# Kernel optimization log

Measured on AMD Instinct MI355X. Metric: run time of the kernel, lower is better.

## Reference

```python
import jax, jax.numpy as jnp
import numpy as np

Q = 400          # num queries
P = 200000       # num points in event
N_INST = 100     # num GT instances
ALPHA = 0.25     # focal alpha
GAMMA = 2.0      # focal gamma
COST_MASK_W = 1.0
COST_DICE_W = 1.0


def setup_inputs() -> dict:
    key = jax.random.key(0)
    k1, k2 = jax.random.split(key)
    pred_masks = jax.random.normal(k1, (Q, P), dtype=jnp.float32)
    labels = jax.random.randint(k2, (P,), 0, N_INST, dtype=jnp.int64 if jax.config.jax_enable_x64 else jnp.int32)
    return {"pred_masks": pred_masks, "labels": labels, "num_instances": N_INST}


def reference(pred_masks, labels, num_instances):
    # pred_masks: [Q, P] mask logits; labels: [P] instance ids in [0, num_instances)
    x = pred_masks.astype(jnp.float32)
    p = jax.nn.sigmoid(x)                      # [Q, P]
    log_p = jax.nn.log_sigmoid(x)              # log sigmoid(x), stable
    log_1mp = jax.nn.log_sigmoid(-x)           # log(1 - sigmoid(x)), stable

    # Focal BCE per point, split by binary target value t in {0,1}:
    #   t=1: alpha     * (1-p)^gamma * (-log p)
    #   t=0: (1-alpha) *    p^gamma  * (-log(1-p))
    f1 = -ALPHA * (1.0 - p) ** GAMMA * log_p        # [Q, P]
    f0 = -(1.0 - ALPHA) * p ** GAMMA * log_1mp      # [Q, P]

    # One-hot GT masks per instance: T[p, j] = 1 iff labels[p] == j
    T = jax.nn.one_hot(labels, num_instances, dtype=jnp.float32)  # [P, N]

    # cost_mask[q, j] = mean_p [ T[p,j]*f1[q,p] + (1-T[p,j])*f0[q,p] ]
    #                 = ( (f1 - f0) @ T + sum_p f0 ) / P   -- avoids [Q,N,P]
    Pn = jnp.asarray(x.shape[1], dtype=jnp.float32)
    cost_mask = (jnp.einsum('qp,pj->qj', f1 - f0, T) + f0.sum(-1, keepdims=True)) / Pn

    # Dice cost (same einsum form as the torch code)
    counts = T.sum(0)                                # [N] points per instance
    numerator = 2.0 * jnp.einsum('qp,pj->qj', p, T)  # [Q, N]
    denominator = p.sum(-1)[:, None] + counts[None, :]
    cost_dice = 1.0 - (numerator + 1.0) / (denominator + 1.0)

    return COST_MASK_W * cost_mask + COST_DICE_W * cost_dice  # [Q, N]
```

## Files before the change

### kernel.cpp

```cpp
#include <hip/hip_runtime.h>
#include <hip/hip_bf16.h>
#include <cstdint>


#define FOCAL_ALPHA 0.25f
constexpr int NMAX   = 128;
constexpr int NTILES = 7;
constexpr int BLOCK  = 256;
constexpr int KC     = 110;

typedef __attribute__((ext_vector_type(8))) short short8;
typedef __attribute__((ext_vector_type(4))) float f32x4;

__device__ __forceinline__ void point_math(float x, float& d, float& f0o, float& po) {
    float e  = __expf(-x);
    float a  = 1.0f + e;
    float p  = __builtin_amdgcn_rcpf(a);
    float l  = __logf(a);
    float lm = -x - l;
    float om = e * p;
    float f1 = FOCAL_ALPHA * (om * om) * l;
    float f0 = -(1.0f - FOCAL_ALPHA) * (p * p) * lm;
    d   = f1 - f0;
    f0o = f0;
    po  = p;
}

__device__ __forceinline__ uint32_t pack_bf16_trunc(float lo, float hi) {
    return __builtin_amdgcn_perm(__float_as_uint(hi), __float_as_uint(lo), 0x07060302u);
}

__global__ __launch_bounds__(256) void
build_B(const int* __restrict__ labels, uint4* __restrict__ Bpre, int steps) {
    int tid  = blockIdx.x * 256 + threadIdx.x;
    int step = tid >> 6;
    int lane = tid & 63;
    if (step >= steps) return;
    const int quad = lane >> 4;
    const int m    = lane & 15;
    const int base = step * 32 + quad * 8;
    int4 l0 = *(const int4*)(labels + base);
    int4 l1 = *(const int4*)(labels + base + 4);
    int ls[8] = {l0.x, l0.y, l0.z, l0.w, l1.x, l1.y, l1.z, l1.w};
    #pragma unroll
    for (int t = 0; t < NTILES; ++t) {
        const int tgt = t * 16 + m;
        uint32_t u[4];
        #pragma unroll
        for (int i = 0; i < 4; ++i) {
            uint32_t lo = (ls[2*i]   == tgt) ? 0x00003F80u : 0u;
            uint32_t hi = (ls[2*i+1] == tgt) ? 0x3F800000u : 0u;
            u[i] = lo | hi;
        }
        Bpre[((size_t)step * NTILES + t) * 64 + lane] = make_uint4(u[0], u[1], u[2], u[3]);
    }
}

union BU { uint4 q; short8 v; uint32_t u[4]; };

__global__ __launch_bounds__(BLOCK) void
matcher_main_pre(const float* __restrict__ pred, const uint4* __restrict__ Bpre,
                 float* __restrict__ S1, float* __restrict__ S2,
                 float* __restrict__ sumf0, float* __restrict__ sump,
                 int Q, int P, int N) {
    const int tid  = threadIdx.x;
    const int wave = tid >> 6;
    const int lane = tid & 63;
    const int m    = lane & 15;
    const int quad = lane >> 4;

    const int strip = blockIdx.y * 4 + wave;
    const int q0    = strip * 16;
    if (q0 >= Q) return;

    const int total_steps = P >> 5;
    const int per         = (total_steps + KC - 1) / KC;
    const int s0          = blockIdx.x * per;
    const int s1          = min(s0 + per, total_steps);
    if (s0 >= s1) return;

    const float* pr = pred + (size_t)(q0 + m) * P + quad * 8 + s0 * 32;
    const uint4* bp = Bpre + (size_t)s0 * (NTILES * 64) + lane;

    f32x4 c1[NTILES], c2[NTILES];
    #pragma unroll
    for (int t = 0; t < NTILES; ++t) {
        c1[t] = (f32x4){0.f, 0.f, 0.f, 0.f};
        c2[t] = (f32x4){0.f, 0.f, 0.f, 0.f};
    }
    float sf0 = 0.0f, sp = 0.0f;

    float4 cx0 = *(const float4*)pr;
    float4 cx1 = *(const float4*)(pr + 4);
    BU cb[NTILES];
    #pragma unroll
    for (int t = 0; t < NTILES; ++t) cb[t].q = bp[t * 64];

    for (int s = s0; s < s1; ++s) {
        pr += 32; bp += NTILES * 64;
        float4 nx0, nx1; BU nb[NTILES];
        if (s + 1 < s1) {
            nx0 = *(const float4*)pr;
            nx1 = *(const float4*)(pr + 4);
            #pragma unroll
            for (int t = 0; t < NTILES; ++t) nb[t].q = bp[t * 64];
        }

        float xs[8] = {cx0.x, cx0.y, cx0.z, cx0.w, cx1.x, cx1.y, cx1.z, cx1.w};
        float v[8], pv[8];
        #pragma unroll
        for (int j = 0; j < 8; ++j) {
            float f0j;
            point_math(xs[j], v[j], f0j, pv[j]);
            sf0 += f0j;
            sp  += pv[j];
        }

        BU A1, A2;
        #pragma unroll
        for (int i = 0; i < 4; ++i) {
            A1.u[i] = pack_bf16_trunc(v[2*i],  v[2*i+1]);
            A2.u[i] = pack_bf16_trunc(pv[2*i], pv[2*i+1]);
        }

        #pragma unroll
        for (int t = 0; t < NTILES; ++t) {
            c1[t] = __builtin_amdgcn_mfma_f32_16x16x32_bf16(A1.v, cb[t].v, c1[t], 0, 0, 0);
            c2[t] = __builtin_amdgcn_mfma_f32_16x16x32_bf16(A2.v, cb[t].v, c2[t], 0, 0, 0);
        }

        cx0 = nx0; cx1 = nx1;
        #pragma unroll
        for (int t = 0; t < NTILES; ++t) cb[t] = nb[t];
    }

    sf0 += __shfl_xor(sf0, 16, 64);
    sf0 += __shfl_xor(sf0, 32, 64);
    sp  += __shfl_xor(sp, 16, 64);
    sp  += __shfl_xor(sp, 32, 64);
    if (lane < 16) {
        unsafeAtomicAdd(&sumf0[q0 + lane], sf0);
        unsafeAtomicAdd(&sump[q0 + lane], sp);
    }

    #pragma unroll
    for (int t = 0; t < NTILES; ++t) {
        const int col = t * 16 + m;
        if (col < N) {
            #pragma unroll
            for (int r = 0; r < 4; ++r) {
                const int row = q0 + quad * 4 + r;
                unsafeAtomicAdd(&S1[(size_t)row * N + col], c1[t][r]);
                unsafeAtomicAdd(&S2[(size_t)row * N + col], c2[t][r]);
            }
        }
    }
}

__global__ __launch_bounds__(BLOCK) void
matcher_main_fly(const float* __restrict__ pred, const int* __restrict__ labels,
                 float* __restrict__ S1, float* __restrict__ S2,
                 float* __restrict__ sumf0, float* __restrict__ sump,
                 int Q, int P, int N) {
    const int tid  = threadIdx.x;
    const int wave = tid >> 6;
    const int lane = tid & 63;
    const int m    = lane & 15;
    const int quad = lane >> 4;

    const int strip = blockIdx.y * 4 + wave;
    const int q0    = strip * 16;
    if (q0 >= Q) return;

    const int total_steps = P >> 5;
    const int per         = (total_steps + KC - 1) / KC;
    const int s0          = blockIdx.x * per;
    const int s1          = min(s0 + per, total_steps);
    if (s0 >= s1) return;

    const float* pr = pred + (size_t)(q0 + m) * P + quad * 8 + s0 * 32;
    const int*   lr = labels + quad * 8 + s0 * 32;

    f32x4 c1[NTILES], c2[NTILES];
    #pragma unroll
    for (int t = 0; t < NTILES; ++t) {
        c1[t] = (f32x4){0.f, 0.f, 0.f, 0.f};
        c2[t] = (f32x4){0.f, 0.f, 0.f, 0.f};
    }
    float sf0 = 0.0f, sp = 0.0f;

    float4 cx0 = *(const float4*)pr;
    float4 cx1 = *(const float4*)(pr + 4);
    int4   cl0 = *(const int4*)lr;
    int4   cl1 = *(const int4*)(lr + 4);

    for (int s = s0; s < s1; ++s) {
        pr += 32; lr += 32;
        float4 nx0, nx1; int4 nl0, nl1;
        if (s + 1 < s1) {
            nx0 = *(const float4*)pr;
            nx1 = *(const float4*)(pr + 4);
            nl0 = *(const int4*)lr;
            nl1 = *(const int4*)(lr + 4);
        }

        float xs[8] = {cx0.x, cx0.y, cx0.z, cx0.w, cx1.x, cx1.y, cx1.z, cx1.w};
        int   ls[8] = {cl0.x, cl0.y, cl0.z, cl0.w, cl1.x, cl1.y, cl1.z, cl1.w};
        float v[8], pv[8];
        #pragma unroll
        for (int j = 0; j < 8; ++j) {
            float f0j;
            point_math(xs[j], v[j], f0j, pv[j]);
            sf0 += f0j;
            sp  += pv[j];
        }

        BU A1, A2;
        #pragma unroll
        for (int i = 0; i < 4; ++i) {
            A1.u[i] = pack_bf16_trunc(v[2*i],  v[2*i+1]);
            A2.u[i] = pack_bf16_trunc(pv[2*i], pv[2*i+1]);
        }

        #pragma unroll
        for (int t = 0; t < NTILES; ++t) {
            const int tgt = t * 16 + m;
            BU B;
            #pragma unroll
            for (int i = 0; i < 4; ++i) {
                uint32_t lo = (ls[2*i]   == tgt) ? 0x00003F80u : 0u;
                uint32_t hi = (ls[2*i+1] == tgt) ? 0x3F800000u : 0u;
                B.u[i] = lo | hi;
            }
            c1[t] = __builtin_amdgcn_mfma_f32_16x16x32_bf16(A1.v, B.v, c1[t], 0, 0, 0);
            c2[t] = __builtin_amdgcn_mfma_f32_16x16x32_bf16(A2.v, B.v, c2[t], 0, 0, 0);
        }

        cx0 = nx0; cx1 = nx1; cl0 = nl0; cl1 = nl1;
    }

    sf0 += __shfl_xor(sf0, 16, 64);
    sf0 += __shfl_xor(sf0, 32, 64);
    sp  += __shfl_xor(sp, 16, 64);
    sp  += __shfl_xor(sp, 32, 64);
    if (lane < 16) {
        unsafeAtomicAdd(&sumf0[q0 + lane], sf0);
        unsafeAtomicAdd(&sump[q0 + lane], sp);
    }

    #pragma unroll
    for (int t = 0; t < NTILES; ++t) {
        const int col = t * 16 + m;
        if (col < N) {
            #pragma unroll
            for (int r = 0; r < 4; ++r) {
                const int row = q0 + quad * 4 + r;
                unsafeAtomicAdd(&S1[(size_t)row * N + col], c1[t][r]);
                unsafeAtomicAdd(&S2[(size_t)row * N + col], c2[t][r]);
            }
        }
    }
}

__global__ __launch_bounds__(256) void
matcher_counts(const int* __restrict__ labels, int* __restrict__ counts, int P, int N) {
    __shared__ int c[NMAX];
    for (int i = threadIdx.x; i < NMAX; i += 256) c[i] = 0;
    __syncthreads();
    const int stride = gridDim.x * 256;
    for (int i = blockIdx.x * 256 + threadIdx.x; i < P; i += stride)
        atomicAdd(&c[labels[i]], 1);
    __syncthreads();
    for (int j = threadIdx.x; j < N; j += 256)
        if (c[j] != 0) atomicAdd(&counts[j], c[j]);
}

__global__ __launch_bounds__(256) void
matcher_final(const float* __restrict__ S1, const float* __restrict__ S2,
              const float* __restrict__ sumf0, const float* __restrict__ sump,
              const int* __restrict__ counts, float* __restrict__ out,
              int Q, int P, int N) {
    int idx = blockIdx.x * 256 + threadIdx.x;
    if (idx >= Q * N) return;
    int q = idx / N;
    int j = idx - q * N;
    float invP = 1.0f / (float)P;
    float cost_mask = (S1[idx] + sumf0[q]) * invP;
    float cost_dice = 1.0f - (2.0f * S2[idx] + 1.0f) / (sump[q] + (float)counts[j] + 1.0f);
    out[idx] = cost_mask + cost_dice;
}

extern "C" void kernel_launch(void* const* d_in, const int* in_sizes, int n_in,
                              void* d_out, int out_size, void* d_ws, size_t ws_size,
                              hipStream_t stream) {
    const float* pred   = (const float*)d_in[0];
    const int*   labels = (const int*)d_in[1];
    const int P = in_sizes[1];
    const int Q = in_sizes[0] / P;
    const int N = out_size / Q;

    float* S1     = (float*)d_ws;
    float* S2     = S1 + (size_t)Q * N;
    float* sumf0  = S2 + (size_t)Q * N;
    float* sump   = sumf0 + Q;
    int*   counts = (int*)(sump + Q);
    size_t base_bytes = ((size_t)2 * Q * N + 2 * Q + N) * sizeof(float);

    const int steps = P >> 5;
    size_t bpre_off   = (base_bytes + 255) & ~(size_t)255;
    size_t bpre_bytes = (size_t)steps * NTILES * 64 * sizeof(uint4);
    bool use_pre = (ws_size >= bpre_off + bpre_bytes);

    hipMemsetAsync(d_ws, 0, base_bytes, stream);
    matcher_counts<<<64, 256, 0, stream>>>(labels, counts, P, N);

    const int strips = (Q + 15) / 16;
    dim3 grid(KC, (strips + 3) / 4);

    if (use_pre) {
        uint4* Bpre = (uint4*)((char*)d_ws + bpre_off);
        build_B<<<(steps * 64 + 255) / 256, 256, 0, stream>>>(labels, Bpre, steps);
        matcher_main_pre<<<grid, BLOCK, 0, stream>>>(pred, Bpre, S1, S2, sumf0, sump, Q, P, N);
    } else {
        matcher_main_fly<<<grid, BLOCK, 0, stream>>>(pred, labels, S1, S2, sumf0, sump, Q, P, N);
    }

    int qn = Q * N;
    matcher_final<<<(qn + 255) / 256, 256, 0, stream>>>(S1, S2, sumf0, sump, counts,
                                                        (float*)d_out, Q, P, N);
}
```

Measured before the change: 550.8 us.

## Build one-hot B tiles cooperatively in shared memory instead of global precompute

Drops the separate build_B pass and its large global B buffer. Each block now builds the one-hot bf16 B fragments for the current step in double-buffered LDS, with each wave computing one or two tiles and a __syncthreads per step. This removes the global write and re-read of the precomputed B (about 50 MB) and the per-wave redundant label compares. It also raises KC from 110 to 146 and adds a launch-bounds occupancy hint, at the cost of a block barrier every step.

```diff
diff --git a/kernel.cpp b/kernel.cpp
--- a/kernel.cpp
+++ b/kernel.cpp
@@ -1,5 +1,4 @@
 #include <hip/hip_runtime.h>
-#include <hip/hip_bf16.h>
 #include <cstdint>
 
 
@@ -7,10 +6,12 @@
 constexpr int NMAX   = 128;
 constexpr int NTILES = 7;
 constexpr int BLOCK  = 256;
-constexpr int KC     = 110;
+constexpr int KC     = 146;
 
 typedef __attribute__((ext_vector_type(8))) short short8;
 typedef __attribute__((ext_vector_type(4))) float f32x4;
+
+union BU { uint4 q; short8 v; uint32_t u[4]; };
 
 __device__ __forceinline__ void point_math(float x, float& d, float& f0o, float& po) {
     float e  = __expf(-x);
@@ -30,39 +31,13 @@
     return __builtin_amdgcn_perm(__float_as_uint(hi), __float_as_uint(lo), 0x07060302u);
 }
 
-__global__ __launch_bounds__(256) void
-build_B(const int* __restrict__ labels, uint4* __restrict__ Bpre, int steps) {
-    int tid  = blockIdx.x * 256 + threadIdx.x;
-    int step = tid >> 6;
-    int lane = tid & 63;
-    if (step >= steps) return;
-    const int quad = lane >> 4;
-    const int m    = lane & 15;
-    const int base = step * 32 + quad * 8;
-    int4 l0 = *(const int4*)(labels + base);
-    int4 l1 = *(const int4*)(labels + base + 4);
-    int ls[8] = {l0.x, l0.y, l0.z, l0.w, l1.x, l1.y, l1.z, l1.w};
-    #pragma unroll
-    for (int t = 0; t < NTILES; ++t) {
-        const int tgt = t * 16 + m;
-        uint32_t u[4];
-        #pragma unroll
-        for (int i = 0; i < 4; ++i) {
-            uint32_t lo = (ls[2*i]   == tgt) ? 0x00003F80u : 0u;
-            uint32_t hi = (ls[2*i+1] == tgt) ? 0x3F800000u : 0u;
-            u[i] = lo | hi;
-        }
-        Bpre[((size_t)step * NTILES + t) * 64 + lane] = make_uint4(u[0], u[1], u[2], u[3]);
-    }
-}
-
-union BU { uint4 q; short8 v; uint32_t u[4]; };
-
-__global__ __launch_bounds__(BLOCK) void
-matcher_main_pre(const float* __restrict__ pred, const uint4* __restrict__ Bpre,
-                 float* __restrict__ S1, float* __restrict__ S2,
-                 float* __restrict__ sumf0, float* __restrict__ sump,
-                 int Q, int P, int N) {
+__global__ __launch_bounds__(BLOCK, 4) void
+matcher_main(const float* __restrict__ pred, const int* __restrict__ labels,
+             float* __restrict__ S1, float* __restrict__ S2,
+             float* __restrict__ sumf0, float* __restrict__ sump,
+             int Q, int P, int N) {
+    __shared__ uint4 Bl[2][NTILES][64];
+
     const int tid  = threadIdx.x;
     const int wave = tid >> 6;
     const int lane = tid & 63;
@@ -71,7 +46,7 @@
 
     const int strip = blockIdx.y * 4 + wave;
     const int q0    = strip * 16;
-    if (q0 >= Q) return;
+    const bool alive = (q0 < Q);
 
     const int total_steps = P >> 5;
     const int per         = (total_steps + KC - 1) / KC;
@@ -79,8 +54,14 @@
     const int s1          = min(s0 + per, total_steps);
     if (s0 >= s1) return;
 
-    const float* pr = pred + (size_t)(q0 + m) * P + quad * 8 + s0 * 32;
-    const uint4* bp = Bpre + (size_t)s0 * (NTILES * 64) + lane;
+    const int  t0   = wave;
+    const int  t1   = wave + 4;
+    const bool has2 = (t1 < NTILES);
+    const int  tgt0 = t0 * 16 + m;
+    const int  tgt1 = t1 * 16 + m;
+
+    const int*   lr = labels + (size_t)s0 * 32 + quad * 8;
+    const float* pr = pred + (size_t)(q0 + m) * P + quad * 8 + (size_t)s0 * 32;
 
     f32x4 c1[NTILES], c2[NTILES];
     #pragma unroll
@@ -90,173 +71,100 @@
     }
     float sf0 = 0.0f, sp = 0.0f;
 
-    float4 cx0 = *(const float4*)pr;
-    float4 cx1 = *(const float4*)(pr + 4);
-    BU cb[NTILES];
-    #pragma unroll
-    for (int t = 0; t < NTILES; ++t) cb[t].q = bp[t * 64];
-
-    for (int s = s0; s < s1; ++s) {
-        pr += 32; bp += NTILES * 64;
-        float4 nx0, nx1; BU nb[NTILES];
-        if (s + 1 < s1) {
-            nx0 = *(const float4*)pr;
-            nx1 = *(const float4*)(pr + 4);
-            #pragma unroll
-            for (int t = 0; t < NTILES; ++t) nb[t].q = bp[t * 64];
-        }
-
-        float xs[8] = {cx0.x, cx0.y, cx0.z, cx0.w, cx1.x, cx1.y, cx1.z, cx1.w};
-        float v[8], pv[8];
-        #pragma unroll
-        for (int j = 0; j < 8; ++j) {
-            float f0j;
-            point_math(xs[j], v[j], f0j, pv[j]);
-            sf0 += f0j;
-            sp  += pv[j];
-        }
-
-        BU A1, A2;
+    auto build = [&](const int* lp, int buf) {
+        int4 l0 = *(const int4*)lp;
+        int4 l1 = *(const int4*)(lp + 4);
+        const int ls[8] = {l0.x, l0.y, l0.z, l0.w, l1.x, l1.y, l1.z, l1.w};
+        BU B0;
         #pragma unroll
         for (int i = 0; i < 4; ++i) {
-            A1.u[i] = pack_bf16_trunc(v[2*i],  v[2*i+1]);
-            A2.u[i] = pack_bf16_trunc(pv[2*i], pv[2*i+1]);
+            uint32_t lo = (ls[2*i]   == tgt0) ? 0x00003F80u : 0u;
+            uint32_t hi = (ls[2*i+1] == tgt0) ? 0x3F800000u : 0u;
+            B0.u[i] = lo | hi;
+        }
+        Bl[buf][t0][lane] = B0.q;
+        if (has2) {
+            BU B1;
+            #pragma unroll
+            for (int i = 0; i < 4; ++i) {
+                uint32_t lo = (ls[2*i]   == tgt1) ? 0x00003F80u : 0u;
+                uint32_t hi = (ls[2*i+1] == tgt1) ? 0x3F800000u : 0u;
+                B1.u[i] = lo | hi;
+            }
+            Bl[buf][t1][lane] = B1.q;
+        }
+    };
+
+    float4 cx0, cx1;
+    if (alive) {
+        cx0 = *(const float4*)pr;
+        cx1 = *(const float4*)(pr + 4);
+    }
+    build(lr, 0);
+    __syncthreads();
+
+    for (int s = s0; s < s1; ++s) {
+        const int  ph   = (s - s0) & 1;
+        const bool more = (s + 1 < s1);
+
+        lr += 32;
+        if (more) build(lr, ph ^ 1);
+
+        if (alive) {
+            float4 nx0, nx1;
+            if (more) {
+                nx0 = *(const float4*)(pr + 32);
+                nx1 = *(const float4*)(pr + 36);
+            }
+
+            const float xs[8] = {cx0.x, cx0.y, cx0.z, cx0.w,
+                                 cx1.x, cx1.y, cx1.z, cx1.w};
+            BU A1, A2;
+            #pragma unroll
+            for (int i = 0; i < 4; ++i) {
+                float d0, f0a, p0, d1, f0b, p1;
+                point_math(xs[2*i],     d0, f0a, p0);
+                point_math(xs[2*i + 1], d1, f0b, p1);
+                sf0 += f0a + f0b;
+                sp  += p0 + p1;
+                A1.u[i] = pack_bf16_trunc(d0, d1);
+                A2.u[i] = pack_bf16_trunc(p0, p1);
+            }
+
+            #pragma unroll
+            for (int t = 0; t < NTILES; ++t) {
+                BU B;
+                B.q = Bl[ph][t][lane];
+                c1[t] = __builtin_amdgcn_mfma_f32_16x16x32_bf16(A1.v, B.v, c1[t], 0, 0, 0);
+                c2[t] = __builtin_amdgcn_mfma_f32_16x16x32_bf16(A2.v, B.v, c2[t], 0, 0, 0);
+            }
+            pr += 32;
+            cx0 = nx0; cx1 = nx1;
+        }
+        __syncthreads();
+    }
+
+    if (alive) {
+        float a = sf0, b = sp;
+        a += __shfl_xor(a, 16, 64);
+        a += __shfl_xor(a, 32, 64);
+        b += __shfl_xor(b, 16, 64);
+        b += __shfl_xor(b, 32, 64);
+        if (lane < 16) {
+            unsafeAtomicAdd(&sumf0[q0 + lane], a);
+            unsafeAtomicAdd(&sump[q0 + lane], b);
         }
 
         #pragma unroll
         for (int t = 0; t < NTILES; ++t) {
-            c1[t] = __builtin_amdgcn_mfma_f32_16x16x32_bf16(A1.v, cb[t].v, c1[t], 0, 0, 0);
-            c2[t] = __builtin_amdgcn_mfma_f32_16x16x32_bf16(A2.v, cb[t].v, c2[t], 0, 0, 0);
-        }
-
-        cx0 = nx0; cx1 = nx1;
-        #pragma unroll
-        for (int t = 0; t < NTILES; ++t) cb[t] = nb[t];
-    }
-
-    sf0 += __shfl_xor(sf0, 16, 64);
-    sf0 += __shfl_xor(sf0, 32, 64);
-    sp  += __shfl_xor(sp, 16, 64);
-    sp  += __shfl_xor(sp, 32, 64);
-    if (lane < 16) {
-        unsafeAtomicAdd(&sumf0[q0 + lane], sf0);
-        unsafeAtomicAdd(&sump[q0 + lane], sp);
-    }
-
-    #pragma unroll
-    for (int t = 0; t < NTILES; ++t) {
-        const int col = t * 16 + m;
-        if (col < N) {
-            #pragma unroll
-            for (int r = 0; r < 4; ++r) {
-                const int row = q0 + quad * 4 + r;
-                unsafeAtomicAdd(&S1[(size_t)row * N + col], c1[t][r]);
-                unsafeAtomicAdd(&S2[(size_t)row * N + col], c2[t][r]);
-            }
-        }
-    }
-}
-
-__global__ __launch_bounds__(BLOCK) void
-matcher_main_fly(const float* __restrict__ pred, const int* __restrict__ labels,
-                 float* __restrict__ S1, float* __restrict__ S2,
-                 float* __restrict__ sumf0, float* __restrict__ sump,
-                 int Q, int P, int N) {
-    const int tid  = threadIdx.x;
-    const int wave = tid >> 6;
-    const int lane = tid & 63;
-    const int m    = lane & 15;
-    const int quad = lane >> 4;
-
-    const int strip = blockIdx.y * 4 + wave;
-    const int q0    = strip * 16;
-    if (q0 >= Q) return;
-
-    const int total_steps = P >> 5;
-    const int per         = (total_steps + KC - 1) / KC;
-    const int s0          = blockIdx.x * per;
-    const int s1          = min(s0 + per, total_steps);
-    if (s0 >= s1) return;
-
-    const float* pr = pred + (size_t)(q0 + m) * P + quad * 8 + s0 * 32;
-    const int*   lr = labels + quad * 8 + s0 * 32;
-
-    f32x4 c1[NTILES], c2[NTILES];
-    #pragma unroll
-    for (int t = 0; t < NTILES; ++t) {
-        c1[t] = (f32x4){0.f, 0.f, 0.f, 0.f};
-        c2[t] = (f32x4){0.f, 0.f, 0.f, 0.f};
-    }
-    float sf0 = 0.0f, sp = 0.0f;
-
-    float4 cx0 = *(const float4*)pr;
-    float4 cx1 = *(const float4*)(pr + 4);
-    int4   cl0 = *(const int4*)lr;
-    int4   cl1 = *(const int4*)(lr + 4);
-
-    for (int s = s0; s < s1; ++s) {
-        pr += 32; lr += 32;
-        float4 nx0, nx1; int4 nl0, nl1;
-        if (s + 1 < s1) {
-            nx0 = *(const float4*)pr;
-            nx1 = *(const float4*)(pr + 4);
-            nl0 = *(const int4*)lr;
-            nl1 = *(const int4*)(lr + 4);
-        }
-
-        float xs[8] = {cx0.x, cx0.y, cx0.z, cx0.w, cx1.x, cx1.y, cx1.z, cx1.w};
-        int   ls[8] = {cl0.x, cl0.y, cl0.z, cl0.w, cl1.x, cl1.y, cl1.z, cl1.w};
-        float v[8], pv[8];
-        #pragma unroll
-        for (int j = 0; j < 8; ++j) {
-            float f0j;
-            point_math(xs[j], v[j], f0j, pv[j]);
-            sf0 += f0j;
-            sp  += pv[j];
-        }
-
-        BU A1, A2;
-        #pragma unroll
-        for (int i = 0; i < 4; ++i) {
-            A1.u[i] = pack_bf16_trunc(v[2*i],  v[2*i+1]);
-            A2.u[i] = pack_bf16_trunc(pv[2*i], pv[2*i+1]);
-        }
-
-        #pragma unroll
-        for (int t = 0; t < NTILES; ++t) {
-            const int tgt = t * 16 + m;
-            BU B;
-            #pragma unroll
-            for (int i = 0; i < 4; ++i) {
-                uint32_t lo = (ls[2*i]   == tgt) ? 0x00003F80u : 0u;
-                uint32_t hi = (ls[2*i+1] == tgt) ? 0x3F800000u : 0u;
-                B.u[i] = lo | hi;
-            }
-            c1[t] = __builtin_amdgcn_mfma_f32_16x16x32_bf16(A1.v, B.v, c1[t], 0, 0, 0);
-            c2[t] = __builtin_amdgcn_mfma_f32_16x16x32_bf16(A2.v, B.v, c2[t], 0, 0, 0);
-        }
-
-        cx0 = nx0; cx1 = nx1; cl0 = nl0; cl1 = nl1;
-    }
-
-    sf0 += __shfl_xor(sf0, 16, 64);
-    sf0 += __shfl_xor(sf0, 32, 64);
-    sp  += __shfl_xor(sp, 16, 64);
-    sp  += __shfl_xor(sp, 32, 64);
-    if (lane < 16) {
-        unsafeAtomicAdd(&sumf0[q0 + lane], sf0);
-        unsafeAtomicAdd(&sump[q0 + lane], sp);
-    }
-
-    #pragma unroll
-    for (int t = 0; t < NTILES; ++t) {
-        const int col = t * 16 + m;
-        if (col < N) {
-            #pragma unroll
-            for (int r = 0; r < 4; ++r) {
-                const int row = q0 + quad * 4 + r;
-                unsafeAtomicAdd(&S1[(size_t)row * N + col], c1[t][r]);
-                unsafeAtomicAdd(&S2[(size_t)row * N + col], c2[t][r]);
+            const int col = t * 16 + m;
+            if (col < N) {
+                #pragma unroll
+                for (int r = 0; r < 4; ++r) {
+                    const int row = q0 + quad * 4 + r;
+                    unsafeAtomicAdd(&S1[(size_t)row * N + col], c1[t][r]);
+                    unsafeAtomicAdd(&S2[(size_t)row * N + col], c2[t][r]);
+                }
             }
         }
     }
@@ -306,24 +214,12 @@
     int*   counts = (int*)(sump + Q);
     size_t base_bytes = ((size_t)2 * Q * N + 2 * Q + N) * sizeof(float);
 
-    const int steps = P >> 5;
-    size_t bpre_off   = (base_bytes + 255) & ~(size_t)255;
-    size_t bpre_bytes = (size_t)steps * NTILES * 64 * sizeof(uint4);
-    bool use_pre = (ws_size >= bpre_off + bpre_bytes);
-
     hipMemsetAsync(d_ws, 0, base_bytes, stream);
     matcher_counts<<<64, 256, 0, stream>>>(labels, counts, P, N);
 
     const int strips = (Q + 15) / 16;
     dim3 grid(KC, (strips + 3) / 4);
-
-    if (use_pre) {
-        uint4* Bpre = (uint4*)((char*)d_ws + bpre_off);
-        build_B<<<(steps * 64 + 255) / 256, 256, 0, stream>>>(labels, Bpre, steps);
-        matcher_main_pre<<<grid, BLOCK, 0, stream>>>(pred, Bpre, S1, S2, sumf0, sump, Q, P, N);
-    } else {
-        matcher_main_fly<<<grid, BLOCK, 0, stream>>>(pred, labels, S1, S2, sumf0, sump, Q, P, N);
-    }
+    matcher_main<<<grid, BLOCK, 0, stream>>>(pred, labels, S1, S2, sumf0, sump, Q, P, N);
 
     int qn = Q * N;
     matcher_final<<<(qn + 255) / 256, 256, 0, stream>>>(S1, S2, sumf0, sump, counts,
```

After: 517.0 us. -6.1%, faster.
